# Kernel optimization log

Measured on AMD Instinct MI355X. Metric: run time of the kernel, lower is better.

Reference implementation:

```python
import jax, jax.numpy as jnp
import numpy as np

IN_CH = 128
NUM_GROUPS = 32
EPS = 1e-5


def group_norm(x, weight, bias):
    b, c, h, w = x.shape
    g = NUM_GROUPS
    xg = x.reshape(b, g, c // g, h, w)
    mean = xg.mean(axis=(2, 3, 4), keepdims=True)
    var = xg.var(axis=(2, 3, 4), keepdims=True)
    xg = (xg - mean) * jax.lax.rsqrt(var + EPS)
    x = xg.reshape(b, c, h, w)
    return x * weight[None, :, None, None] + bias[None, :, None, None]


def conv1x1(x, w, b):
    # x: (b,c,h,w), w: (out,in), b: (out,)
    return jnp.einsum('oc,bchw->bohw', w, x) + b[None, :, None, None]


def setup_inputs() -> dict:
    key = jax.random.key(0)
    ks = jax.random.split(key, 6)
    b, c, h, w = 8, IN_CH, 64, 64
    scale = 1.0 / np.sqrt(c)  # xavier-ish scale for 1x1 convs
    return {
        'x': jax.random.normal(ks[0], (b, c, h, w), dtype=jnp.float32),
        'gn_weight': jnp.ones((c,), dtype=jnp.float32),
        'gn_bias': jnp.zeros((c,), dtype=jnp.float32),
        'wq': jax.random.normal(ks[1], (c, c), dtype=jnp.float32) * scale,
        'bq': jnp.zeros((c,), dtype=jnp.float32),
        'wk': jax.random.normal(ks[2], (c, c), dtype=jnp.float32) * scale,
        'bk': jnp.zeros((c,), dtype=jnp.float32),
        'wv': jax.random.normal(ks[3], (c, c), dtype=jnp.float32) * scale,
        'bv': jnp.zeros((c,), dtype=jnp.float32),
        'wo': jax.random.normal(ks[4], (c, c), dtype=jnp.float32) * scale,
        'bo': jnp.zeros((c,), dtype=jnp.float32),
        'gamma': jnp.ones((1,), dtype=jnp.float32),
    }


def reference(x, gn_weight, gn_bias, wq, bq, wk, bk, wv, bv, wo, bo, gamma):
    b, c, h, w = x.shape
    x_dash = group_norm(x, gn_weight, gn_bias)
    q = conv1x1(x_dash, wq, bq).reshape(b, c, h * w)  # (b,c,n)
    k = conv1x1(x_dash, wk, bk).reshape(b, c, h * w)
    v = conv1x1(x_dash, wv, bv).reshape(b, c, h * w)
    # attn[b,i,j] = sum_c q[b,c,i] k[b,c,j] / sqrt(c)
    attn = jnp.einsum('bci,bcj->bij', q, k) / jnp.sqrt(jnp.float32(c))
    attn = jax.nn.softmax(attn, axis=-1)
    # out[b,c,i] = sum_j v[b,c,j] attn[b,i,j]
    out = jnp.einsum('bcj,bij->bci', v, attn).reshape(b, c, h, w)
    out = conv1x1(out, wo, bo)
    return x + gamma[0] * out
```

## Files before the change

### kernel.cpp

```cpp
#include <hip/hip_runtime.h>

typedef unsigned short u16;
typedef unsigned int u32;
typedef __bf16 bf16_t;
typedef bf16_t bf16x8 __attribute__((ext_vector_type(8)));
typedef float f32x4 __attribute__((ext_vector_type(4)));
typedef u32 u32x4 __attribute__((ext_vector_type(4)));

#define BATCH 8
#define CH 128
#define NSP 4096
#define LOG2E 1.44269504088896f

static __device__ __forceinline__ u16 f2bf(float f) {
  u32 u = __builtin_bit_cast(u32, f);
  u32 r = u + 0x7FFFu + ((u >> 16) & 1u);
  return (u16)(r >> 16);
}

static __device__ __forceinline__ bf16x8 ld_bf8(const u16* p) {
  return __builtin_bit_cast(bf16x8, *(const u32x4*)p);
}

static __device__ __forceinline__ f32x4 mfma16(bf16x8 a, bf16x8 b, f32x4 c) {
  return __builtin_amdgcn_mfma_f32_16x16x32_bf16(a, b, c, 0, 0, 0);
}

static __device__ __forceinline__ u32 cvt_pk(float lo, float hi) {
  u32 r;
  asm("v_cvt_pk_bf16_f32 %0, %1, %2" : "=v"(r) : "v"(lo), "v"(hi));
  return r;
}

static __device__ __forceinline__ float fast_exp2(float x) {
#if __has_builtin(__builtin_amdgcn_exp2f)
  return __builtin_amdgcn_exp2f(x);
#else
  return exp2f(x);
#endif
}

static __device__ __forceinline__ void gl2lds16(const u16* g, u16* l) {
  __builtin_amdgcn_global_load_lds((const __attribute__((address_space(1))) void*)g,
                                   (__attribute__((address_space(3))) void*)l, 16, 0, 0);
}

__global__ __launch_bounds__(256) void gn_stats_kernel(const float* __restrict__ x,
                                                       float* __restrict__ stats,
                                                       const float* __restrict__ wq,
                                                       const float* __restrict__ wk,
                                                       const float* __restrict__ wv,
                                                       const float* __restrict__ wo,
                                                       u16* __restrict__ wbf) {
  int bg = blockIdx.x;
  {
    int widx = bg * 256 + threadIdx.x;
    int m = widx >> 14, r = widx & 16383;
    const float* s = (m == 0) ? wq : (m == 1) ? wk : (m == 2) ? wv : wo;
    wbf[widx] = f2bf(s[r]);
  }
  const float4* p = (const float4*)(x + (size_t)bg * 16384);
  float s = 0.f, ss = 0.f;
  for (int i = threadIdx.x; i < 4096; i += 256) {
    float4 v = p[i];
    s += v.x + v.y + v.z + v.w;
    ss += v.x * v.x + v.y * v.y + v.z * v.z + v.w * v.w;
  }
  for (int off = 32; off; off >>= 1) {
    s += __shfl_xor(s, off);
    ss += __shfl_xor(ss, off);
  }
  __shared__ float rs[4], rss[4];
  int wave = threadIdx.x >> 6;
  if ((threadIdx.x & 63) == 0) { rs[wave] = s; rss[wave] = ss; }
  __syncthreads();
  if (threadIdx.x == 0) {
    s = rs[0] + rs[1] + rs[2] + rs[3];
    ss = rss[0] + rss[1] + rss[2] + rss[3];
    float mean = s * (1.f / 16384.f);
    float var = ss * (1.f / 16384.f) - mean * mean;
    stats[2 * bg] = mean;
    stats[2 * bg + 1] = rsqrtf(var + 1e-5f);
  }
}

__global__ __launch_bounds__(256) void qkv_kernel(const float* __restrict__ x,
                                                  const float* __restrict__ stats,
                                                  const float* __restrict__ gnw,
                                                  const float* __restrict__ gnb,
                                                  const u16* __restrict__ wqb,
                                                  const u16* __restrict__ wkb,
                                                  const u16* __restrict__ wvb,
                                                  const float* __restrict__ bq,
                                                  const float* __restrict__ bk,
                                                  const float* __restrict__ bv,
                                                  u16* __restrict__ q, u16* __restrict__ k,
                                                  u16* __restrict__ v) {
  __shared__ float tile[64][132];
  __shared__ float sc[128], sh[128];
  int b = blockIdx.y;
  int n0 = blockIdx.x * 64;
  int t = threadIdx.x;
  if (t < 128) {
    float mean = stats[2 * (b * 32 + (t >> 2))];
    float rstd = stats[2 * (b * 32 + (t >> 2)) + 1];
    float w = gnw[t];
    sc[t] = rstd * w;
    sh[t] = gnb[t] - mean * rstd * w;
  }
  __syncthreads();
  const float4* xb4 = (const float4*)(x + (size_t)b * CH * NSP);
#pragma unroll
  for (int i = 0; i < 8; ++i) {
    int idx = t + i * 256;
    int c = idx >> 4, j4 = idx & 15;
    float4 vv = xb4[(size_t)c * (NSP / 4) + (n0 >> 2) + j4];
    float s_ = sc[c], h_ = sh[c];
    tile[j4 * 4 + 0][c] = vv.x * s_ + h_;
    tile[j4 * 4 + 1][c] = vv.y * s_ + h_;
    tile[j4 * 4 + 2][c] = vv.z * s_ + h_;
    tile[j4 * 4 + 3][c] = vv.w * s_ + h_;
  }
  __syncthreads();

  int wave = t >> 6, lane = t & 63;
  int lr = lane & 15, lg = lane >> 4;
  int n_base = n0 + wave * 16;
  int row = wave * 16 + lr;

  bf16x8 xfr[4];
#pragma unroll
  for (int kk = 0; kk < 4; ++kk) {
    const float* p = &tile[row][kk * 32 + lg * 8];
    f32x4 lo = *(const f32x4*)p;
    f32x4 hi = *(const f32x4*)(p + 4);
    u32x4 xw = {cvt_pk(lo[0], lo[1]), cvt_pk(lo[2], lo[3]),
                cvt_pk(hi[0], hi[1]), cvt_pk(hi[2], hi[3])};
    xfr[kk] = __builtin_bit_cast(bf16x8, xw);
  }

  f32x4 accq[8] = {}, acck[8] = {}, accv[8] = {};
#pragma unroll
  for (int kk = 0; kk < 4; ++kk) {
    int coff = kk * 32 + lg * 8;
    bf16x8 xa = xfr[kk];
#pragma unroll
    for (int ot = 0; ot < 8; ++ot) {
      int woff = (ot * 16 + lr) * CH + coff;
      bf16x8 wqf = ld_bf8(wqb + woff);
      bf16x8 wkf = ld_bf8(wkb + woff);
      bf16x8 wvf = ld_bf8(wvb + woff);
      accq[ot] = mfma16(xa, wqf, accq[ot]);
      acck[ot] = mfma16(xa, wkf, acck[ot]);
      accv[ot] = mfma16(wvf, xa, accv[ot]);
    }
  }
  const float qscale = 0.08838834764831845f * LOG2E;
  int jj = wave * 16 + lr;
  int frv = (jj >> 5) * 4 + ((jj & 15) >> 2);
  int ev = (lr & 3) + ((wave & 1) << 2);
#pragma unroll
  for (int ot = 0; ot < 8; ++ot) {
    int o_col = ot * 16 + lr;
    float bqv = bq[o_col], bkv = bk[o_col];
#pragma unroll
    for (int r = 0; r < 4; ++r) {
      int nrow = n_base + lg * 4 + r;
      q[((size_t)b * NSP + nrow) * CH + o_col] = f2bf((accq[ot][r] + bqv) * qscale);
      int cperm = ((((o_col >> 3) ^ (nrow & 7)) << 3)) | (o_col & 7);
      k[((size_t)b * NSP + nrow) * CH + cperm] = f2bf(acck[ot][r] + bkv);
    }
#pragma unroll
    for (int r = 0; r < 4; ++r) {
      int c = ot * 16 + lg * 4 + r;
      int slot = frv ^ (c & 7);
      v[((size_t)(b * CH + c)) * NSP + blockIdx.x * 64 + slot * 8 + ev] =
          f2bf(accv[ot][r] + bv[c]);
    }
  }
}

__global__ __launch_bounds__(256, 2) void attn_kernel(const u16* __restrict__ q,
                                                      const u16* __restrict__ k,
                                                      const u16* __restrict__ v,
                                                      u16* __restrict__ part0,
                                                      u16* __restrict__ part1,
                                                      float* __restrict__ lbuf) {
  __shared__ __align__(16) u16 kbuf[2][64 * 128];
  __shared__ __align__(16) u16 vbuf[2][128 * 64];
  int id = blockIdx.x;
  int b = id & 7;
  int qblk = (id >> 3) & 31;
  int split = id >> 8;
  int wave = threadIdx.x >> 6, lane = threadIdx.x & 63;
  int lr = lane & 15, lg = lane >> 4;
  int i_base = qblk * 128 + wave * 32;
  int t0 = split * 32, t1 = t0 + 32;

  const u16* kg = k + (size_t)b * NSP * CH;
  const u16* vg = v + (size_t)b * CH * NSP;

  bf16x8 qa[2][4];
#pragma unroll
  for (int qt = 0; qt < 2; ++qt) {
    const u16* qrow = q + ((size_t)b * NSP + i_base + qt * 16 + lr) * CH;
#pragma unroll
    for (int kk = 0; kk < 4; ++kk) qa[qt][kk] = ld_bf8(qrow + kk * 32 + lg * 8);
  }

  auto STAGEK = [&](int t, int bi) {
    const u16* src = kg + ((size_t)(t * 64 + wave * 16)) * CH + lane * 8;
    u16* dst = &kbuf[bi][wave * 16 * 128];
#pragma unroll
    for (int g = 0; g < 4; ++g) gl2lds16(src + g * 512, dst + g * 512);
  };
  int vco = wave * 32 + (lane >> 3);
  auto STAGEV = [&](int t, int bi) {
    const u16* src = vg + t * 64 + (lane & 7) * 8;
    u16* dst = &vbuf[bi][wave * 32 * 64];
#pragma unroll
    for (int g = 0; g < 4; ++g) gl2lds16(src + (size_t)(vco + g * 8) * NSP, dst + g * 512);
  };

  STAGEK(t0, 0);
  STAGEV(t0, 0);

  const u32x4 ones_u = {0x3F803F80u, 0x3F803F80u, 0x3F803F80u, 0x3F803F80u};
  const bf16x8 ones = __builtin_bit_cast(bf16x8, ones_u);

  f32x4 oacc[2][8] = {};
  f32x4 lacc[2] = {};

  for (int t = t0; t < t1; ++t) {
    int cur = (t - t0) & 1;
    const u16* kb = kbuf[cur];
    const u16* vb = vbuf[cur];
    asm volatile("s_waitcnt vmcnt(0)" ::: "memory");
    __builtin_amdgcn_s_barrier();
    __builtin_amdgcn_sched_barrier(0);
    if (t + 1 < t1) STAGEK(t + 1, cur ^ 1);

    f32x4 s[2][4] = {};
    __builtin_amdgcn_s_setprio(1);
#pragma unroll
    for (int kk = 0; kk < 4; ++kk) {
#pragma unroll
      for (int jt = 0; jt < 4; ++jt) {
        int row = jt * 16 + lr;
        bf16x8 kf = ld_bf8(kb + row * 128 + ((((kk << 2) + lg) ^ (row & 7)) << 3));
        s[0][jt] = mfma16(kf, qa[0][kk], s[0][jt]);
        s[1][jt] = mfma16(kf, qa[1][kk], s[1][jt]);
      }
    }
    __builtin_amdgcn_s_setprio(0);
    if (t + 1 < t1) STAGEV(t + 1, cur ^ 1);

#pragma unroll
    for (int kk2 = 0; kk2 < 2; ++kk2) {
      u32x4 paw[2];
#pragma unroll
      for (int qt = 0; qt < 2; ++qt) {
        float p0 = fast_exp2(s[qt][2 * kk2][0]);
        float p1 = fast_exp2(s[qt][2 * kk2][1]);
        float p2 = fast_exp2(s[qt][2 * kk2][2]);
        float p3 = fast_exp2(s[qt][2 * kk2][3]);
        float p4 = fast_exp2(s[qt][2 * kk2 + 1][0]);
        float p5 = fast_exp2(s[qt][2 * kk2 + 1][1]);
        float p6 = fast_exp2(s[qt][2 * kk2 + 1][2]);
        float p7 = fast_exp2(s[qt][2 * kk2 + 1][3]);
        paw[qt][0] = cvt_pk(p0, p1);
        paw[qt][1] = cvt_pk(p2, p3);
        paw[qt][2] = cvt_pk(p4, p5);
        paw[qt][3] = cvt_pk(p6, p7);
      }
      bf16x8 pa0 = __builtin_bit_cast(bf16x8, paw[0]);
      bf16x8 pa1 = __builtin_bit_cast(bf16x8, paw[1]);
      __builtin_amdgcn_s_setprio(1);
      lacc[0] = mfma16(pa0, ones, lacc[0]);
      lacc[1] = mfma16(pa1, ones, lacc[1]);
#pragma unroll
      for (int ct = 0; ct < 8; ++ct) {
        int c = ct * 16 + lr;
        bf16x8 vf = ld_bf8(vb + c * 64 + ((((kk2 << 2) + lg) ^ (c & 7)) << 3));
        oacc[0][ct] = mfma16(pa0, vf, oacc[0][ct]);
        oacc[1][ct] = mfma16(pa1, vf, oacc[1][ct]);
      }
      __builtin_amdgcn_s_setprio(0);
    }
  }

  u16* pdst = (split == 0) ? part0 : part1;
  float* ldst = lbuf + (size_t)split * (BATCH * NSP) + (size_t)b * NSP;
#pragma unroll
  for (int qt = 0; qt < 2; ++qt) {
#pragma unroll
    for (int r = 0; r < 4; ++r) {
      int i = i_base + qt * 16 + lg * 4 + r;
      if (lr == 0) ldst[i] = lacc[qt][r];
      u16* row = pdst + ((size_t)b * NSP + i) * CH;
#pragma unroll
      for (int ct = 0; ct < 8; ++ct) row[ct * 16 + lr] = f2bf(oacc[qt][ct][r]);
    }
  }
}

__global__ __launch_bounds__(256) void proj_kernel(const u16* __restrict__ p0,
                                                   const u16* __restrict__ p1,
                                                   const float* __restrict__ lbuf,
                                                   const u16* __restrict__ wob,
                                                   const float* __restrict__ bo,
                                                   const float* __restrict__ gamma,
                                                   const float* __restrict__ x,
                                                   float* __restrict__ out) {
  int b = blockIdx.y;
  int wave = threadIdx.x >> 6, lane = threadIdx.x & 63;
  int lr = lane & 15, lg = lane >> 4;
  int n_base = blockIdx.x * 64 + wave * 16;
  int nrow = n_base + lr;
  float linv = 1.f / (lbuf[(size_t)b * NSP + nrow] +
                      lbuf[(size_t)BATCH * NSP + (size_t)b * NSP + nrow]);
  const u16* r0 = p0 + ((size_t)b * NSP + nrow) * CH;
  const u16* r1 = p1 + ((size_t)b * NSP + nrow) * CH;
  f32x4 acc[8] = {};
#pragma unroll
  for (int kk = 0; kk < 4; ++kk) {
    int coff = kk * 32 + lg * 8;
    bf16x8 a = ld_bf8(r0 + coff);
    bf16x8 bb = ld_bf8(r1 + coff);
    u32 w0 = cvt_pk(((float)a[0] + (float)bb[0]) * linv, ((float)a[1] + (float)bb[1]) * linv);
    u32 w1 = cvt_pk(((float)a[2] + (float)bb[2]) * linv, ((float)a[3] + (float)bb[3]) * linv);
    u32 w2 = cvt_pk(((float)a[4] + (float)bb[4]) * linv, ((float)a[5] + (float)bb[5]) * linv);
    u32 w3 = cvt_pk(((float)a[6] + (float)bb[6]) * linv, ((float)a[7] + (float)bb[7]) * linv);
    u32x4 wv = {w0, w1, w2, w3};
    bf16x8 ofrag = __builtin_bit_cast(bf16x8, wv);
#pragma unroll
    for (int ot = 0; ot < 8; ++ot) {
      bf16x8 wf = ld_bf8(wob + (ot * 16 + lr) * CH + coff);
      acc[ot] = mfma16(wf, ofrag, acc[ot]);
    }
  }
  float g = gamma[0];
  int n_col = n_base + lr;
#pragma unroll
  for (int ot = 0; ot < 8; ++ot) {
#pragma unroll
    for (int r = 0; r < 4; ++r) {
      int o_row = ot * 16 + lg * 4 + r;
      size_t off = ((size_t)b * CH + o_row) * NSP + n_col;
      out[off] = x[off] + g * (acc[ot][r] + bo[o_row]);
    }
  }
}

extern "C" void kernel_launch(void* const* d_in, const int* in_sizes, int n_in,
                              void* d_out, int out_size, void* d_ws, size_t ws_size,
                              hipStream_t stream) {
  const float* x = (const float*)d_in[0];
  const float* gnw = (const float*)d_in[1];
  const float* gnb = (const float*)d_in[2];
  const float* wq = (const float*)d_in[3];
  const float* bq = (const float*)d_in[4];
  const float* wk = (const float*)d_in[5];
  const float* bk = (const float*)d_in[6];
  const float* wv = (const float*)d_in[7];
  const float* bv = (const float*)d_in[8];
  const float* wo = (const float*)d_in[9];
  const float* bo = (const float*)d_in[10];
  const float* gamma = (const float*)d_in[11];
  float* out = (float*)d_out;

  const size_t BUF = (size_t)BATCH * NSP * CH * sizeof(u16);
  char* ws = (char*)d_ws;
  u16* wbf = (u16*)ws;
  float* stats = (float*)(ws + 131072);
  u16* xd = (u16*)(ws + 262144);
  u16* qb = (u16*)(ws + 262144 + BUF);
  u16* kb = (u16*)(ws + 262144 + 2 * BUF);
  u16* vb = (u16*)(ws + 262144 + 3 * BUF);
  float* lbuf = (float*)(ws + 262144 + 4 * BUF);
  const size_t need = 262144 + 4 * BUF + 262144;
  if (ws_size < need) return;
  u16* part1 = (ws_size >= need + BUF) ? (u16*)(ws + need) : qb;

  gn_stats_kernel<<<256, 256, 0, stream>>>(x, stats, wq, wk, wv, wo, wbf);
  qkv_kernel<<<dim3(64, 8), 256, 0, stream>>>(x, stats, gnw, gnb, wbf, wbf + 16384,
                                              wbf + 32768, bq, bk, bv, qb, kb, vb);
  attn_kernel<<<512, 256, 0, stream>>>(qb, kb, vb, xd, part1, lbuf);
  proj_kernel<<<dim3(64, 8), 256, 0, stream>>>(xd, part1, lbuf, wbf + 49152, bo, gamma,
                                               x, out);
}
```

Measured before the change: 127.4 us.

## Stage QKV weights through LDS and compute Q, K, V sequentially

The QKV projection kernel now copies each 128x128 bf16 weight matrix into shared memory (reusing the x tile buffer) with swizzled direct global-to-LDS loads. Previously every wave read weight fragments straight from global memory. Q, K and V are now computed one after another with a single accumulator set, which lowers register pressure. In exchange there are extra barriers and serialized load waits between the three phases.

```diff
diff --git a/kernel.cpp b/kernel.cpp
--- a/kernel.cpp
+++ b/kernel.cpp
@@ -96,8 +96,10 @@
                                                   const float* __restrict__ bv,
                                                   u16* __restrict__ q, u16* __restrict__ k,
                                                   u16* __restrict__ v) {
-  __shared__ float tile[64][132];
+  __shared__ __align__(16) char smem[64 * 132 * 4];
   __shared__ float sc[128], sh[128];
+  float(*tile)[132] = (float(*)[132])smem;
+  u16* wbuf = (u16*)smem;
   int b = blockIdx.y;
   int n0 = blockIdx.x * 64;
   int t = threadIdx.x;
@@ -138,44 +140,89 @@
                 cvt_pk(hi[0], hi[1]), cvt_pk(hi[2], hi[3])};
     xfr[kk] = __builtin_bit_cast(bf16x8, xw);
   }
-
-  f32x4 accq[8] = {}, acck[8] = {}, accv[8] = {};
-#pragma unroll
-  for (int kk = 0; kk < 4; ++kk) {
-    int coff = kk * 32 + lg * 8;
-    bf16x8 xa = xfr[kk];
+  __syncthreads();
+
+  auto STAGEW = [&](const u16* w) {
+#pragma unroll
+    for (int g = 0; g < 8; ++g) {
+      int wr = wave * 32 + g * 4 + (lane >> 4);
+      gl2lds16(w + wr * CH + (((lane & 15) ^ (wr & 7)) << 3),
+               wbuf + (wave * 32 + g * 4) * 128);
+    }
+  };
+  auto WFRAG = [&](int ot, int kk) {
+    int wr = ot * 16 + lr;
+    return ld_bf8(wbuf + wr * 128 + ((((kk << 2) + lg) ^ (wr & 7)) << 3));
+  };
+
+  const float qscale = 0.08838834764831845f * LOG2E;
+
+  STAGEW(wqb);
+  asm volatile("s_waitcnt vmcnt(0)" ::: "memory");
+  __syncthreads();
+  {
+    f32x4 acc[8] = {};
+#pragma unroll
+    for (int kk = 0; kk < 4; ++kk)
+#pragma unroll
+      for (int ot = 0; ot < 8; ++ot) acc[ot] = mfma16(xfr[kk], WFRAG(ot, kk), acc[ot]);
 #pragma unroll
     for (int ot = 0; ot < 8; ++ot) {
-      int woff = (ot * 16 + lr) * CH + coff;
-      bf16x8 wqf = ld_bf8(wqb + woff);
-      bf16x8 wkf = ld_bf8(wkb + woff);
-      bf16x8 wvf = ld_bf8(wvb + woff);
-      accq[ot] = mfma16(xa, wqf, accq[ot]);
-      acck[ot] = mfma16(xa, wkf, acck[ot]);
-      accv[ot] = mfma16(wvf, xa, accv[ot]);
-    }
-  }
-  const float qscale = 0.08838834764831845f * LOG2E;
-  int jj = wave * 16 + lr;
-  int frv = (jj >> 5) * 4 + ((jj & 15) >> 2);
-  int ev = (lr & 3) + ((wave & 1) << 2);
-#pragma unroll
-  for (int ot = 0; ot < 8; ++ot) {
-    int o_col = ot * 16 + lr;
-    float bqv = bq[o_col], bkv = bk[o_col];
-#pragma unroll
-    for (int r = 0; r < 4; ++r) {
-      int nrow = n_base + lg * 4 + r;
-      q[((size_t)b * NSP + nrow) * CH + o_col] = f2bf((accq[ot][r] + bqv) * qscale);
-      int cperm = ((((o_col >> 3) ^ (nrow & 7)) << 3)) | (o_col & 7);
-      k[((size_t)b * NSP + nrow) * CH + cperm] = f2bf(acck[ot][r] + bkv);
-    }
-#pragma unroll
-    for (int r = 0; r < 4; ++r) {
-      int c = ot * 16 + lg * 4 + r;
-      int slot = frv ^ (c & 7);
-      v[((size_t)(b * CH + c)) * NSP + blockIdx.x * 64 + slot * 8 + ev] =
-          f2bf(accv[ot][r] + bv[c]);
+      int o_col = ot * 16 + lr;
+      float bqv = bq[o_col];
+#pragma unroll
+      for (int r = 0; r < 4; ++r) {
+        int nrow = n_base + lg * 4 + r;
+        q[((size_t)b * NSP + nrow) * CH + o_col] = f2bf((acc[ot][r] + bqv) * qscale);
+      }
+    }
+  }
+  __syncthreads();
+
+  STAGEW(wkb);
+  asm volatile("s_waitcnt vmcnt(0)" ::: "memory");
+  __syncthreads();
+  {
+    f32x4 acc[8] = {};
+#pragma unroll
+    for (int kk = 0; kk < 4; ++kk)
+#pragma unroll
+      for (int ot = 0; ot < 8; ++ot) acc[ot] = mfma16(xfr[kk], WFRAG(ot, kk), acc[ot]);
+#pragma unroll
+    for (int ot = 0; ot < 8; ++ot) {
+      int o_col = ot * 16 + lr;
+      float bkv = bk[o_col];
+#pragma unroll
+      for (int r = 0; r < 4; ++r) {
+        int nrow = n_base + lg * 4 + r;
+        int cperm = ((((o_col >> 3) ^ (nrow & 7)) << 3)) | (o_col & 7);
+        k[((size_t)b * NSP + nrow) * CH + cperm] = f2bf(acc[ot][r] + bkv);
+      }
+    }
+  }
+  __syncthreads();
+
+  STAGEW(wvb);
+  asm volatile("s_waitcnt vmcnt(0)" ::: "memory");
+  __syncthreads();
+  {
+    f32x4 acc[8] = {};
+#pragma unroll
+    for (int kk = 0; kk < 4; ++kk)
+#pragma unroll
+      for (int ot = 0; ot < 8; ++ot) acc[ot] = mfma16(WFRAG(ot, kk), xfr[kk], acc[ot]);
+    int jj = wave * 16 + lr;
+    int frv = (jj >> 5) * 4 + ((jj & 15) >> 2);
+    int ev = (lr & 3) + ((wave & 1) << 2);
+#pragma unroll
+    for (int ot = 0; ot < 8; ++ot) {
+#pragma unroll
+      for (int r = 0; r < 4; ++r) {
+        int c = ot * 16 + lg * 4 + r;
+        int slot = frv ^ (c & 7);
+        v[((size_t)(b * CH + c)) * NSP + blockIdx.x * 64 + slot * 8 + ev] =
+            f2bf(acc[ot][r] + bv[c]);
+      }
     }
   }
 }
```

Measured after the change: 111.3 us. 1.14x faster.
